# Optimization experiments

Hardware: AMD Instinct MI355X
Metric: run time of the kernel (lower is better)

The kernel has to match this reference:

```python
import jax, jax.numpy as jnp
import numpy as np

N = 100000
E = 3200000
IN_DIM, HID_DIM, OUT_DIM = 29, 64, 2


def setup_inputs() -> dict:
    key = jax.random.key(0)
    k1, k2, k3, k4, k5 = jax.random.split(key, 5)
    x = jax.random.normal(k1, (N, IN_DIM), dtype=jnp.float32)
    edge_index = jax.random.randint(k2, (2, E), 0, N, dtype=jnp.int64)
    # GCNConv params: glorot-ish weights, zero bias (bias added after aggregation)
    W1 = jax.random.normal(k3, (IN_DIM, HID_DIM), dtype=jnp.float32) * (1.0 / np.sqrt(IN_DIM))
    b1 = jnp.zeros((HID_DIM,), dtype=jnp.float32)
    W2 = jax.random.normal(k4, (HID_DIM, OUT_DIM), dtype=jnp.float32) * (1.0 / np.sqrt(HID_DIM))
    b2 = jnp.zeros((OUT_DIM,), dtype=jnp.float32)
    return {"x": x, "edge_index": edge_index, "W1": W1, "b1": b1, "W2": W2, "b2": b2}


def _gcn_norm(edge_index, n_nodes):
    # PyG gcn_norm with add_self_loops=True, symmetric D^-1/2 A D^-1/2
    loop = jnp.arange(n_nodes, dtype=edge_index.dtype)
    src = jnp.concatenate([edge_index[0], loop])
    dst = jnp.concatenate([edge_index[1], loop])
    deg = jax.ops.segment_sum(jnp.ones_like(dst, dtype=jnp.float32), dst, num_segments=n_nodes)
    dinv = jnp.where(deg > 0, jax.lax.rsqrt(deg), 0.0)
    norm = dinv[src] * dinv[dst]  # [E + N]
    return src, dst, norm


def _gcn_conv(x, src, dst, norm, W, b):
    h = x @ W                      # [N, d_out] -- transform first (smaller msgs)
    msg = h[src] * norm[:, None]   # [E+N, d_out] gather + scale
    out = jax.ops.segment_sum(msg, dst, num_segments=x.shape[0])  # scatter-add
    return out + b


def reference(x, edge_index, W1, b1, W2, b2):
    src, dst, norm = _gcn_norm(edge_index, x.shape[0])
    h = _gcn_conv(x, src, dst, norm, W1, b1)
    h = jax.nn.relu(h)
    out = _gcn_conv(h, src, dst, norm, W2, b2)
    return out
```

## Files before the change

kernel.cpp:

```cpp
#include <hip/hip_runtime.h>

#define N_NODES 100000
#define N_EDGES 3200000
#define IN_DIM  29
#define HID_DIM 64
#define NBUCK   391
#define BNODES  256
#define CAP     10240
#define EPT     8
#define EPB     4096

#define OFF_CUR   0
#define OFF_ROWS  512
#define OFF_ROWE  100512
#define OFF_DINV  200512
#define OFF_ZS    300512
#define OFF_EBUF  500512
#define OFF_XS    4504352

static __device__ __forceinline__ unsigned short f2bf(float f) {
    unsigned u = __float_as_uint(f);
    u += 0x7fffu + ((u >> 16) & 1u);
    return (unsigned short)(u >> 16);
}

static __device__ __forceinline__ void unpack_add(float4& acc, uint2 a) {
    acc.x += __uint_as_float(a.x << 16);
    acc.y += __uint_as_float(a.x & 0xFFFF0000u);
    acc.z += __uint_as_float(a.y << 16);
    acc.w += __uint_as_float(a.y & 0xFFFF0000u);
}

__global__ __launch_bounds__(512) void partition_kernel(const int* __restrict__ ei,
        int* __restrict__ gcursor, int* __restrict__ ebuf) {
    __shared__ int lhist[NBUCK];
    __shared__ int lcur[NBUCK];
    int tid = threadIdx.x;
    for (int i = tid; i < NBUCK; i += 512) lhist[i] = 0;
    __syncthreads();

    int base = blockIdx.x * EPB + tid * EPT;
    int dv[EPT], sv[EPT];
    bool valid = (base < N_EDGES);
    if (valid) {
        const int4* dp = (const int4*)(ei + N_EDGES + base);
        const int4* sp = (const int4*)(ei + base);
        #pragma unroll
        for (int q = 0; q < 2; ++q) {
            int4 t = dp[q];
            dv[4*q+0] = t.x; dv[4*q+1] = t.y; dv[4*q+2] = t.z; dv[4*q+3] = t.w;
            int4 u = sp[q];
            sv[4*q+0] = u.x; sv[4*q+1] = u.y; sv[4*q+2] = u.z; sv[4*q+3] = u.w;
        }
        #pragma unroll
        for (int j = 0; j < EPT; ++j) atomicAdd(&lhist[dv[j] >> 8], 1);
    }
    __syncthreads();
    for (int i = tid; i < NBUCK; i += 512) {
        int c = lhist[i];
        lcur[i] = c ? (atomicAdd(&gcursor[i], c) + i * CAP) : 0;
    }
    __syncthreads();
    if (valid) {
        #pragma unroll
        for (int j = 0; j < EPT; ++j) {
            int d = dv[j];
            int pos = atomicAdd(&lcur[d >> 8], 1);
            ebuf[pos] = sv[j] | ((d & 255) << 17);
        }
    }
}

__global__ __launch_bounds__(1024) void bucketsort_kernel(const int* __restrict__ gcursor,
        int* __restrict__ ebuf, int* __restrict__ rowStart, int* __restrict__ rowEnd,
        float* __restrict__ dinv, const float* __restrict__ x,
        unsigned int* __restrict__ xsb) {
    __shared__ int   cnt[BNODES];
    __shared__ int   cur[BNODES];
    __shared__ float dls[BNODES];
    __shared__ int   stage[CAP];
    int b = blockIdx.x, tid = threadIdx.x;
    if (tid < BNODES) cnt[tid] = 0;
    __syncthreads();
    int base = b * CAP;
    int size = gcursor[b];

    for (int j = tid; j < size; j += 1024)
        atomicAdd(&cnt[((unsigned)ebuf[base + j]) >> 17], 1);
    __syncthreads();

    int v = 0;
    if (tid < BNODES) { v = cnt[tid]; cur[tid] = v; }
    __syncthreads();
    for (int off = 1; off < BNODES; off <<= 1) {
        int t = 0;
        if (tid < BNODES && tid >= off) t = cur[tid - off];
        __syncthreads();
        if (tid < BNODES) cur[tid] += t;
        __syncthreads();
    }
    if (tid < BNODES) {
        int excl = cur[tid] - v;
        int node = b * BNODES + tid;
        if (node < N_NODES) {
            rowStart[node] = base + excl;
            rowEnd[node]   = base + excl + v;
            float dn = rsqrtf((float)v + 1.0f);
            dinv[node] = dn;
            dls[tid] = dn;
        }
        cur[tid] = excl;
    }
    __syncthreads();

    for (int j = tid; j < size; j += 1024) {
        unsigned p = (unsigned)ebuf[base + j];
        int pos = atomicAdd(&cur[p >> 17], 1);
        stage[pos] = p & 0x1FFFF;
    }
    __syncthreads();
    for (int j = tid; j < size; j += 1024)
        ebuf[base + j] = stage[j];

    for (int i = tid; i < BNODES * 16; i += 1024) {
        int dl = i >> 4, kp = i & 15;
        int nd = b * BNODES + dl;
        if (nd < N_NODES) {
            float dn = dls[dl];
            int k0 = kp * 2, k1 = k0 + 1;
            float f0 = (k0 < IN_DIM) ? x[nd * IN_DIM + k0] * dn : 0.0f;
            float f1 = (k1 < IN_DIM) ? x[nd * IN_DIM + k1] * dn : 0.0f;
            unsigned u = (unsigned)f2bf(f0) | ((unsigned)f2bf(f1) << 16);
            xsb[(size_t)nd * 16 + kp] = u;
        }
    }
}

__global__ __launch_bounds__(256) void fused_kernel(const unsigned int* __restrict__ xs_,
        const int* __restrict__ rowStart, const int* __restrict__ rowEnd,
        const int* __restrict__ ebuf, const float* __restrict__ dinv,
        const float* __restrict__ W1, const float* __restrict__ b1,
        const float* __restrict__ W2, float* __restrict__ zs) {
    __shared__ float w1s[IN_DIM * HID_DIM];
    __shared__ float b1s[HID_DIM];
    __shared__ float w2s[HID_DIM * 2];
    int tid = threadIdx.x;
    for (int i = tid; i < IN_DIM * HID_DIM; i += 256) w1s[i] = W1[i];
    if (tid < HID_DIM) {
        b1s[tid] = b1[tid];
        w2s[tid * 2 + 0] = W2[tid * 2 + 0];
        w2s[tid * 2 + 1] = W2[tid * 2 + 1];
    }
    __syncthreads();

    int lane = tid & 63;
    int q = lane >> 3, m = lane & 7;
    const uint2* xsb = (const uint2*)xs_;
    int nodeBase = blockIdx.x * 16 + (tid >> 6) * 4;

    for (int rep = 0; rep < 4; ++rep) {
        int node = nodeBase + rep;
        if (node >= N_NODES) break;

        float4 acc = make_float4(0.f, 0.f, 0.f, 0.f);
        if (q == 0)
            unpack_add(acc, xsb[(size_t)node * 8 + m]);

        int rs = rowStart[node], re = rowEnd[node];
        int j = rs + q;
        for (; j + 24 < re; j += 32) {
            int s0 = ebuf[j];
            int s1 = ebuf[j + 8];
            int s2 = ebuf[j + 16];
            int s3 = ebuf[j + 24];
            uint2 a = xsb[(size_t)s0 * 8 + m];
            uint2 bb = xsb[(size_t)s1 * 8 + m];
            uint2 c = xsb[(size_t)s2 * 8 + m];
            uint2 d = xsb[(size_t)s3 * 8 + m];
            unpack_add(acc, a);
            unpack_add(acc, bb);
            unpack_add(acc, c);
            unpack_add(acc, d);
        }
        for (; j < re; j += 8) {
            uint2 a = xsb[(size_t)ebuf[j] * 8 + m];
            unpack_add(acc, a);
        }
        #pragma unroll
        for (int msk = 8; msk <= 32; msk <<= 1) {
            acc.x += __shfl_xor(acc.x, msk);
            acc.y += __shfl_xor(acc.y, msk);
            acc.z += __shfl_xor(acc.z, msk);
            acc.w += __shfl_xor(acc.w, msk);
        }
        float dn = dinv[node];
        acc.x *= dn; acc.y *= dn; acc.z *= dn; acc.w *= dn;

        float h = b1s[lane];
        #pragma unroll
        for (int kk = 0; kk < IN_DIM; ++kk) {
            float comp = ((kk & 3) == 0) ? acc.x : ((kk & 3) == 1) ? acc.y
                       : ((kk & 3) == 2) ? acc.z : acc.w;
            h = fmaf(__shfl(comp, kk >> 2), w1s[kk * HID_DIM + lane], h);
        }
        h = fmaxf(h, 0.0f);

        float z0 = h * w2s[lane * 2 + 0];
        float z1 = h * w2s[lane * 2 + 1];
        #pragma unroll
        for (int off = 32; off > 0; off >>= 1) {
            z0 += __shfl_down(z0, off);
            z1 += __shfl_down(z1, off);
        }
        if (lane == 0) {
            zs[node * 2 + 0] = z0 * dn;
            zs[node * 2 + 1] = z1 * dn;
        }
    }
}

__global__ __launch_bounds__(256) void agg2_kernel(const float* __restrict__ zs,
        const int* __restrict__ rowStart, const int* __restrict__ rowEnd,
        const int* __restrict__ ebuf, const float* __restrict__ dinv,
        const float* __restrict__ b2, float* __restrict__ out) {
    int tid = threadIdx.x;
    int node = blockIdx.x * 16 + (tid >> 4);
    if (node >= N_NODES) return;
    int gl = tid & 15;
    const float2* zs2 = (const float2*)zs;
    float a0 = 0.0f, a1 = 0.0f, c0 = 0.0f, c1 = 0.0f;
    int rs = rowStart[node], re = rowEnd[node];
    int j = rs + gl;
    for (; j + 16 < re; j += 32) {
        float2 za = zs2[ebuf[j]];
        float2 zb = zs2[ebuf[j + 16]];
        a0 += za.x; a1 += za.y;
        c0 += zb.x; c1 += zb.y;
    }
    if (j < re) {
        float2 za = zs2[ebuf[j]];
        a0 += za.x; a1 += za.y;
    }
    a0 += c0; a1 += c1;
    a0 += __shfl_xor(a0, 8); a1 += __shfl_xor(a1, 8);
    a0 += __shfl_xor(a0, 4); a1 += __shfl_xor(a1, 4);
    a0 += __shfl_xor(a0, 2); a1 += __shfl_xor(a1, 2);
    a0 += __shfl_xor(a0, 1); a1 += __shfl_xor(a1, 1);
    if (gl == 0) {
        float dn = dinv[node];
        float2 zself = zs2[node];
        float2 o;
        o.x = dn * (a0 + zself.x) + b2[0];
        o.y = dn * (a1 + zself.y) + b2[1];
        ((float2*)out)[node] = o;
    }
}

extern "C" void kernel_launch(void* const* d_in, const int* in_sizes, int n_in,
                              void* d_out, int out_size, void* d_ws, size_t ws_size,
                              hipStream_t stream) {
    const float* x  = (const float*)d_in[0];
    const int*   ei = (const int*)d_in[1];
    const float* W1 = (const float*)d_in[2];
    const float* b1 = (const float*)d_in[3];
    const float* W2 = (const float*)d_in[4];
    const float* b2 = (const float*)d_in[5];
    float* out = (float*)d_out;

    int*   wsi      = (int*)d_ws;
    float* wsf      = (float*)d_ws;
    int*   gcursor  = wsi + OFF_CUR;
    int*   rowStart = wsi + OFF_ROWS;
    int*   rowEnd   = wsi + OFF_ROWE;
    float* dinv     = wsf + OFF_DINV;
    float* zs       = wsf + OFF_ZS;
    int*   ebuf     = wsi + OFF_EBUF;
    unsigned int* xsb = (unsigned int*)(wsi + OFF_XS);

    hipMemsetAsync(gcursor, 0, NBUCK * sizeof(int), stream);
    partition_kernel<<<(N_EDGES + EPB - 1) / EPB, 512, 0, stream>>>(ei, gcursor, ebuf);
    bucketsort_kernel<<<NBUCK, 1024, 0, stream>>>(gcursor, ebuf, rowStart, rowEnd, dinv, x, xsb);
    fused_kernel<<<(N_NODES + 15) / 16, 256, 0, stream>>>(xsb, rowStart, rowEnd, ebuf, dinv, W1, b1, W2, zs);
    agg2_kernel<<<(N_NODES + 15) / 16, 256, 0, stream>>>(zs, rowStart, rowEnd, ebuf, dinv, b2, out);
}
```

Measured before the change: 227.1 us.

## Halve bucket size, use wave-shuffle scan, and predicate gather tail loops

Doubles the number of destination buckets (128 nodes each, 5120-edge capacity) so the bucket-sort stage launches 782 blocks of 512 threads, which raises occupancy and lowers per-block shared memory. The multi-barrier block-wide prefix scan is replaced by a single-wavefront shuffle scan over pairs of counts. The gather loops in both aggregation kernels drop their separate remainder loops and instead issue all four (or two) loads with clamped indices and predicated accumulation, so the loads stay batched. The trade-off is a few redundant clamped loads on short rows, and each bucket now has less headroom against capacity overflow.

```diff
diff --git a/kernel.cpp b/kernel.cpp
--- a/kernel.cpp
+++ b/kernel.cpp
@@ -4,19 +4,19 @@
 #define N_EDGES 3200000
 #define IN_DIM  29
 #define HID_DIM 64
-#define NBUCK   391
-#define BNODES  256
-#define CAP     10240
+#define NBUCK   782
+#define BNODES  128
+#define CAP     5120
 #define EPT     8
 #define EPB     4096
 
 #define OFF_CUR   0
-#define OFF_ROWS  512
-#define OFF_ROWE  100512
-#define OFF_DINV  200512
-#define OFF_ZS    300512
-#define OFF_EBUF  500512
-#define OFF_XS    4504352
+#define OFF_ROWS  1024
+#define OFF_ROWE  101024
+#define OFF_DINV  201024
+#define OFF_ZS    301024
+#define OFF_EBUF  501024
+#define OFF_XS    4504864
 
 static __device__ __forceinline__ unsigned short f2bf(float f) {
     unsigned u = __float_as_uint(f);
@@ -53,7 +53,7 @@
             sv[4*q+0] = u.x; sv[4*q+1] = u.y; sv[4*q+2] = u.z; sv[4*q+3] = u.w;
         }
         #pragma unroll
-        for (int j = 0; j < EPT; ++j) atomicAdd(&lhist[dv[j] >> 8], 1);
+        for (int j = 0; j < EPT; ++j) atomicAdd(&lhist[dv[j] >> 7], 1);
     }
     __syncthreads();
     for (int i = tid; i < NBUCK; i += 512) {
@@ -65,13 +65,13 @@
         #pragma unroll
         for (int j = 0; j < EPT; ++j) {
             int d = dv[j];
-            int pos = atomicAdd(&lcur[d >> 8], 1);
-            ebuf[pos] = sv[j] | ((d & 255) << 17);
-        }
-    }
-}
-
-__global__ __launch_bounds__(1024) void bucketsort_kernel(const int* __restrict__ gcursor,
+            int pos = atomicAdd(&lcur[d >> 7], 1);
+            ebuf[pos] = sv[j] | ((d & 127) << 17);
+        }
+    }
+}
+
+__global__ __launch_bounds__(512) void bucketsort_kernel(const int* __restrict__ gcursor,
         int* __restrict__ ebuf, int* __restrict__ rowStart, int* __restrict__ rowEnd,
         float* __restrict__ dinv, const float* __restrict__ x,
         unsigned int* __restrict__ xsb) {
@@ -85,22 +85,28 @@
     int base = b * CAP;
     int size = gcursor[b];
 
-    for (int j = tid; j < size; j += 1024)
+    for (int j = tid; j < size; j += 512)
         atomicAdd(&cnt[((unsigned)ebuf[base + j]) >> 17], 1);
     __syncthreads();
 
-    int v = 0;
-    if (tid < BNODES) { v = cnt[tid]; cur[tid] = v; }
-    __syncthreads();
-    for (int off = 1; off < BNODES; off <<= 1) {
-        int t = 0;
-        if (tid < BNODES && tid >= off) t = cur[tid - off];
-        __syncthreads();
-        if (tid < BNODES) cur[tid] += t;
-        __syncthreads();
-    }
+    if (tid < 64) {
+        int a = cnt[2 * tid], bb = cnt[2 * tid + 1];
+        int s = a + bb;
+        int incl = s;
+        #pragma unroll
+        for (int off = 1; off < 64; off <<= 1) {
+            int t = __shfl_up(incl, off);
+            if ((int)tid >= off) incl += t;
+        }
+        int excl = incl - s;
+        cur[2 * tid]     = excl;
+        cur[2 * tid + 1] = excl + a;
+    }
+    __syncthreads();
+
     if (tid < BNODES) {
-        int excl = cur[tid] - v;
+        int v = cnt[tid];
+        int excl = cur[tid];
         int node = b * BNODES + tid;
         if (node < N_NODES) {
             rowStart[node] = base + excl;
@@ -109,20 +115,19 @@
             dinv[node] = dn;
             dls[tid] = dn;
         }
-        cur[tid] = excl;
-    }
-    __syncthreads();
-
-    for (int j = tid; j < size; j += 1024) {
+    }
+    __syncthreads();
+
+    for (int j = tid; j < size; j += 512) {
         unsigned p = (unsigned)ebuf[base + j];
         int pos = atomicAdd(&cur[p >> 17], 1);
         stage[pos] = p & 0x1FFFF;
     }
     __syncthreads();
-    for (int j = tid; j < size; j += 1024)
+    for (int j = tid; j < size; j += 512)
         ebuf[base + j] = stage[j];
 
-    for (int i = tid; i < BNODES * 16; i += 1024) {
+    for (int i = tid; i < BNODES * 16; i += 512) {
         int dl = i >> 4, kp = i & 15;
         int nd = b * BNODES + dl;
         if (nd < N_NODES) {
@@ -167,24 +172,21 @@
             unpack_add(acc, xsb[(size_t)node * 8 + m]);
 
         int rs = rowStart[node], re = rowEnd[node];
-        int j = rs + q;
-        for (; j + 24 < re; j += 32) {
+        int last = re - 1;
+        for (int j = rs + q; j < re; j += 32) {
+            int j1 = j + 8, j2 = j + 16, j3 = j + 24;
             int s0 = ebuf[j];
-            int s1 = ebuf[j + 8];
-            int s2 = ebuf[j + 16];
-            int s3 = ebuf[j + 24];
-            uint2 a = xsb[(size_t)s0 * 8 + m];
+            int s1 = ebuf[min(j1, last)];
+            int s2 = ebuf[min(j2, last)];
+            int s3 = ebuf[min(j3, last)];
+            uint2 a  = xsb[(size_t)s0 * 8 + m];
             uint2 bb = xsb[(size_t)s1 * 8 + m];
-            uint2 c = xsb[(size_t)s2 * 8 + m];
-            uint2 d = xsb[(size_t)s3 * 8 + m];
+            uint2 c  = xsb[(size_t)s2 * 8 + m];
+            uint2 d  = xsb[(size_t)s3 * 8 + m];
             unpack_add(acc, a);
-            unpack_add(acc, bb);
-            unpack_add(acc, c);
-            unpack_add(acc, d);
-        }
-        for (; j < re; j += 8) {
-            uint2 a = xsb[(size_t)ebuf[j] * 8 + m];
-            unpack_add(acc, a);
+            if (j1 < re) unpack_add(acc, bb);
+            if (j2 < re) unpack_add(acc, c);
+            if (j3 < re) unpack_add(acc, d);
         }
         #pragma unroll
         for (int msk = 8; msk <= 32; msk <<= 1) {
@@ -230,16 +232,13 @@
     const float2* zs2 = (const float2*)zs;
     float a0 = 0.0f, a1 = 0.0f, c0 = 0.0f, c1 = 0.0f;
     int rs = rowStart[node], re = rowEnd[node];
-    int j = rs + gl;
-    for (; j + 16 < re; j += 32) {
+    int last = re - 1;
+    for (int j = rs + gl; j < re; j += 32) {
+        int j1 = j + 16;
         float2 za = zs2[ebuf[j]];
-        float2 zb = zs2[ebuf[j + 16]];
+        float2 zb = zs2[ebuf[min(j1, last)]];
         a0 += za.x; a1 += za.y;
-        c0 += zb.x; c1 += zb.y;
-    }
-    if (j < re) {
-        float2 za = zs2[ebuf[j]];
-        a0 += za.x; a1 += za.y;
+        if (j1 < re) { c0 += zb.x; c1 += zb.y; }
     }
     a0 += c0; a1 += c1;
     a0 += __shfl_xor(a0, 8); a1 += __shfl_xor(a1, 8);
@@ -279,7 +278,7 @@
 
     hipMemsetAsync(gcursor, 0, NBUCK * sizeof(int), stream);
     partition_kernel<<<(N_EDGES + EPB - 1) / EPB, 512, 0, stream>>>(ei, gcursor, ebuf);
-    bucketsort_kernel<<<NBUCK, 1024, 0, stream>>>(gcursor, ebuf, rowStart, rowEnd, dinv, x, xsb);
+    bucketsort_kernel<<<NBUCK, 512, 0, stream>>>(gcursor, ebuf, rowStart, rowEnd, dinv, x, xsb);
     fused_kernel<<<(N_NODES + 15) / 16, 256, 0, stream>>>(xsb, rowStart, rowEnd, ebuf, dinv, W1, b1, W2, zs);
     agg2_kernel<<<(N_NODES + 15) / 16, 256, 0, stream>>>(zs, rowStart, rowEnd, ebuf, dinv, b2, out);
 }
```

Result: no change. 229.3 us (+1.0%).
